# Kernel optimization log

Measured on AMD Instinct MI355X. Metric: run time of the kernel, lower is better.

## Reference

```python
import jax, jax.numpy as jnp
import numpy as np
from jax import lax

DT = 0.01  # fixed Euler-Maruyama step size

B, N, C, M, H, T = 1024, 64, 16, 16, 512, 128


def setup_inputs() -> dict:
    key = jax.random.key(0)
    ks = jax.random.split(key, 8)
    d_in = N + C  # concat(y, control)
    inp = {
        "y0": jax.random.normal(ks[0], (B, N), jnp.float32),
        "controls": jax.random.normal(ks[1], (T, C), jnp.float32),
        "noise": jax.random.normal(ks[2], (T - 1, B, M), jnp.float32),
        # mu MLP: d_in -> H -> N
        "W1_mu": jax.random.normal(ks[3], (d_in, H), jnp.float32) / np.sqrt(d_in),
        "b1_mu": jnp.zeros((H,), jnp.float32),
        "W2_mu": jax.random.normal(ks[4], (H, N), jnp.float32) / np.sqrt(H),
        "b2_mu": jnp.zeros((N,), jnp.float32),
        # sigma MLP: d_in -> H -> N*M
        "W1_sg": jax.random.normal(ks[5], (d_in, H), jnp.float32) / np.sqrt(d_in),
        "b1_sg": jnp.zeros((H,), jnp.float32),
        "W2_sg": jax.random.normal(ks[6], (H, N * M), jnp.float32) / np.sqrt(H),
        "b2_sg": jnp.zeros((N * M,), jnp.float32),
    }
    return inp


def _mlp(x, W1, b1, W2, b2):
    return jnp.maximum(x @ W1 + b1, 0.0) @ W2 + b2


def reference(y0, controls, noise, W1_mu, b1_mu, W2_mu, b2_mu,
              W1_sg, b1_sg, W2_sg, b2_sg):
    """Euler-Maruyama solve of dy = f(y,u) dt + g(y,u) dW.
    Returns trajectory [T, B, N] including y0 (as torchsde.sdeint does)."""
    b, n = y0.shape
    m = noise.shape[-1]
    sqrt_dt = jnp.sqrt(jnp.asarray(DT, y0.dtype))

    def step(y, inp):
        u, z = inp  # u: [C] control at t_k, z: [B, M] standard normal
        x = jnp.concatenate([y, jnp.broadcast_to(u[None, :], (b, u.shape[0]))], axis=1)
        drift = _mlp(x, W1_mu, b1_mu, W2_mu, b2_mu)              # [B, N]
        diff = _mlp(x, W1_sg, b1_sg, W2_sg, b2_sg).reshape(b, n, m)  # [B, N, M]
        dW = z * sqrt_dt
        y_next = y + drift * DT + jnp.einsum('bnm,bm->bn', diff, dW)
        return y_next, y_next

    _, ys = lax.scan(step, y0, (controls[:-1], noise))
    return jnp.concatenate([y0[None], ys], axis=0)  # [T, B, N]
```

## Files before the change

### kernel.cpp

```cpp
#include <hip/hip_runtime.h>


typedef _Float16 f16x8 __attribute__((ext_vector_type(8)));
typedef float    f32x4 __attribute__((ext_vector_type(4)));
typedef float    f32x2 __attribute__((ext_vector_type(2)));

#define MFMA(a,b,c) __builtin_amdgcn_mfma_f32_16x16x32_f16(a,b,c,0,0,0)

#define Bb 1024
#define Tt 128
#define NG 64
#define GB 8
#define Rr 16
#define NT 512
#define CNT_STRIDE 16
#define MAGIC1 0x1234ABCDu
#define MAGIC2 0xFEDC4321u

#define W2SG_OFF 0
#define W2SG_HALVES (64*16*2*512)
#define W2MU_OFF (W2SG_OFF + W2SG_HALVES)
#define W2MU_HALVES (4*16*2*512)
#define W1MU_OFF (W2MU_OFF + W2MU_HALVES)
#define W1_HALVES (32*3*2*512)
#define W1SG_OFF (W1MU_OFF + W1_HALVES)
#define WS_HALVES (W1SG_OFF + W1_HALVES)
#define ACC_BYTES_OFF ((size_t)WS_HALVES * 2)
#define ACC_FLOATS (3 * NG * 1024)
#define CNT_OFF   (ACC_BYTES_OFF + (size_t)ACC_FLOATS*4)
#define DTEST_DW  (NG*GB*16)
#define DW16      (NG*16)
#define DET_DW    (DTEST_DW + 6*DW16)
#define WS_END    (CNT_OFF + (size_t)(DW16 + DET_DW)*4)

__global__ __launch_bounds__(256) void pack_weights(
    const float* __restrict__ W1_mu, const float* __restrict__ W2_mu,
    const float* __restrict__ W1_sg, const float* __restrict__ W2_sg,
    _Float16* __restrict__ wsh)
{
    int gid = blockIdx.x * 256 + threadIdx.x;
    if (gid >= 81920) return;
    const float* src; int ncols, kvalid; size_t dst;
    int id, tile, ks, lane;
    if (gid < 65536) {
        id = gid; tile = id >> 10; id &= 1023; ks = id >> 6; lane = id & 63;
        src = W2_sg; ncols = 1024; kvalid = 512;
        dst = W2SG_OFF + (size_t)((tile*16 + ks)*2) * 512 + lane*8;
    } else if (gid < 69632) {
        id = gid - 65536; tile = id >> 10; id &= 1023; ks = id >> 6; lane = id & 63;
        src = W2_mu; ncols = 64; kvalid = 512;
        dst = W2MU_OFF + (size_t)((tile*16 + ks)*2) * 512 + lane*8;
    } else if (gid < 75776) {
        id = gid - 69632; tile = id / 192; id %= 192; ks = id >> 6; lane = id & 63;
        src = W1_mu; ncols = 512; kvalid = 80;
        dst = W1MU_OFF + (size_t)((tile*3 + ks)*2) * 512 + lane*8;
    } else {
        id = gid - 75776; tile = id / 192; id %= 192; ks = id >> 6; lane = id & 63;
        src = W1_sg; ncols = 512; kvalid = 80;
        dst = W1SG_OFF + (size_t)((tile*3 + ks)*2) * 512 + lane*8;
    }
    const int n  = tile*16 + (lane & 15);
    const int kb = ks*32 + ((lane >> 4) << 3);
    f16x8 hi8, lo8;
    #pragma unroll
    for (int jj = 0; jj < 8; ++jj) {
        int k = kb + jj;
        float wv = (k < kvalid) ? src[(size_t)k * ncols + n] : 0.f;
        _Float16 h = (_Float16)wv;
        hi8[jj] = h;
        lo8[jj] = (_Float16)(wv - (float)h);
    }
    *((f16x8*)(wsh + dst))       = hi8;
    *((f16x8*)(wsh + dst + 512)) = lo8;
}

__device__ __forceinline__ unsigned sc0_load_u32(const unsigned* p) {
    unsigned v;
    asm volatile("global_load_dword %0, %1, off sc0\n\ts_waitcnt vmcnt(0)"
                 : "=v"(v) : "v"((const void*)p) : "memory");
    return v;
}

__global__ __launch_bounds__(NT, 4) void nsde_r9(
    const float* __restrict__ y0, const float* __restrict__ controls,
    const float* __restrict__ noise,
    const float* __restrict__ b1_mu, const float* __restrict__ b2_mu,
    const float* __restrict__ b1_sg, const float* __restrict__ b2_sg,
    const _Float16* __restrict__ wf,
    float* __restrict__ accbuf, unsigned int* __restrict__ cnt,
    float* __restrict__ out)
{
    __shared__ _Float16 s_xhi[Rr][104], s_xlo[Rr][104];
    __shared__ _Float16 s_hhi[2][Rr][72], s_hlo[2][Rr][72];
    __shared__ float s_y[Rr*64];
    __shared__ float s_dw[Rr][16];
    __shared__ float s_part[Rr*64];
    __shared__ float s_pmu[Rr*64];
    __shared__ int   s_mode;

    const int tid  = threadIdx.x;
    const int lane = tid & 63, w = tid >> 6;
    const int m15  = lane & 15, quad = lane >> 4;
    const int g    = blockIdx.x & 63;
    const int j    = blockIdx.x >> 6;
    const int r0   = g * Rr;

    unsigned* dtest = cnt + NG*16;
    unsigned* dcntA = dtest + NG*GB*16;
    unsigned* dcntB = dcntA + NG*16;
    unsigned* dtc   = dcntB + NG*16;
    unsigned* dcntC = dtc   + NG*16;
    unsigned* dok   = dcntC + NG*16;
    unsigned* dcnt2 = dok   + NG*16;

    const int l  = w >> 2;
    const int ct = w & 3;
    const int tg = j*4 + ct;
    const _Float16* w1base = wf + (l ? W1SG_OFF : W1MU_OFF);
    const float bias1 = (l ? b1_sg : b1_mu)[j*64 + ct*16 + m15];
    float b2v[8];
    #pragma unroll
    for (int t = 0; t < 8; ++t)
        b2v[t] = (j == 0) ? b2_sg[(w + t*8)*16 + m15] : 0.f;
    const float b2m = (w < 4 && j == 0) ? b2_mu[w*16 + m15] * 0.01f : 0.f;

    if (tid == 0) {
        volatile unsigned* my = (volatile unsigned*)&dtest[(size_t)(g*GB + j)*16];
        int ok = 1;
        *my = MAGIC1;
        asm volatile("s_waitcnt vmcnt(0)" ::: "memory");
        __hip_atomic_fetch_add(&dcntA[g*16], 1u, __ATOMIC_RELEASE,
                               __HIP_MEMORY_SCOPE_AGENT);
        while (__hip_atomic_load(&dcntA[g*16], __ATOMIC_RELAXED,
                                 __HIP_MEMORY_SCOPE_AGENT) < (unsigned)GB)
            __builtin_amdgcn_s_sleep(2);
        for (int b = 0; b < GB; ++b)
            ok &= (sc0_load_u32(&dtest[(size_t)(g*GB + b)*16]) == MAGIC1);
        *my = MAGIC2;
        asm volatile("s_waitcnt vmcnt(0)" ::: "memory");
        __hip_atomic_fetch_add(&dcntB[g*16], 1u, __ATOMIC_RELEASE,
                               __HIP_MEMORY_SCOPE_AGENT);
        while (__hip_atomic_load(&dcntB[g*16], __ATOMIC_RELAXED,
                                 __HIP_MEMORY_SCOPE_AGENT) < (unsigned)GB)
            __builtin_amdgcn_s_sleep(2);
        for (int b = 0; b < GB; ++b)
            ok &= (sc0_load_u32(&dtest[(size_t)(g*GB + b)*16]) == MAGIC2);
        __hip_atomic_fetch_add(&dtc[g*16], 1u, __ATOMIC_RELAXED,
                               __HIP_MEMORY_SCOPE_WORKGROUP);
        asm volatile("s_waitcnt vmcnt(0)" ::: "memory");
        __hip_atomic_fetch_add(&dcntC[g*16], 1u, __ATOMIC_RELEASE,
                               __HIP_MEMORY_SCOPE_AGENT);
        while (__hip_atomic_load(&dcntC[g*16], __ATOMIC_RELAXED,
                                 __HIP_MEMORY_SCOPE_AGENT) < (unsigned)GB)
            __builtin_amdgcn_s_sleep(2);
        ok &= (sc0_load_u32(&dtc[g*16]) == (unsigned)GB);
        __hip_atomic_fetch_add(&dok[g*16], ok ? 1u : 0u, __ATOMIC_RELEASE,
                               __HIP_MEMORY_SCOPE_AGENT);
        __hip_atomic_fetch_add(&dcnt2[g*16], 1u, __ATOMIC_RELEASE,
                               __HIP_MEMORY_SCOPE_AGENT);
        while (__hip_atomic_load(&dcnt2[g*16], __ATOMIC_RELAXED,
                                 __HIP_MEMORY_SCOPE_AGENT) < (unsigned)GB)
            __builtin_amdgcn_s_sleep(2);
        s_mode = (__hip_atomic_load(&dok[g*16], __ATOMIC_RELAXED,
                                    __HIP_MEMORY_SCOPE_AGENT) == (unsigned)GB);
    }
    __syncthreads();
    const bool local = (s_mode != 0);

    for (int e = tid; e < Rr*24; e += NT) {
        int r = e / 24, c = 80 + e % 24;
        s_xhi[r][c] = (_Float16)0.f; s_xlo[r][c] = (_Float16)0.f;
    }
    if (tid < 256) {
        int e0 = tid*4, r = e0 >> 6, n = e0 & 63;
        float4 yv = *(const float4*)&y0[(size_t)(r0 + r)*64 + n];
        float vv[4] = {yv.x, yv.y, yv.z, yv.w};
        #pragma unroll
        for (int q = 0; q < 4; ++q) {
            s_y[e0+q] = vv[q];
            _Float16 h = (_Float16)vv[q];
            s_xhi[r][n+q] = h; s_xlo[r][n+q] = (_Float16)(vv[q] - (float)h);
        }
        if ((tid >> 5) == j)
            *(float4*)&out[(size_t)(r0 + r)*64 + n] = yv;
        int rr2 = tid >> 4, cc2 = tid & 15;
        float u = controls[cc2];
        _Float16 h = (_Float16)u;
        s_xhi[rr2][64+cc2] = h; s_xlo[rr2][64+cc2] = (_Float16)(u - (float)h);
        s_dw[rr2][cc2] = noise[(size_t)(r0 + rr2)*16 + cc2] * 0.1f;
    }
    __syncthreads();

    for (int k = 0; k < Tt-1; ++k) {
        {
            f32x4 a0 = {0,0,0,0}, a1 = {0,0,0,0}, a2 = {0,0,0,0};
            #pragma unroll
            for (int ks = 0; ks < 3; ++ks) {
                const _Float16* bp = w1base + (size_t)((tg*3 + ks)*2)*512 + lane*8;
                f16x8 bh = *(const f16x8*)bp;
                f16x8 bl = *(const f16x8*)(bp + 512);
                f16x8 ah = *(const f16x8*)&s_xhi[m15][ks*32 + quad*8];
                f16x8 al = *(const f16x8*)&s_xlo[m15][ks*32 + quad*8];
                a0 = MFMA(ah, bh, a0);
                a1 = MFMA(ah, bl, a1);
                a2 = MFMA(al, bh, a2);
            }
            f32x4 s = a0 + a1 + a2;
            #pragma unroll
            for (int rg = 0; rg < 4; ++rg) {
                int row = quad*4 + rg;
                float v = fmaxf(s[rg] + bias1, 0.f);
                _Float16 h = (_Float16)v;
                s_hhi[l][row][ct*16 + m15] = h;
                s_hlo[l][row][ct*16 + m15] = (_Float16)(v - (float)h);
            }
        }
        float u_nx = 0.f, dw_nx = 0.f;
        const int r2 = tid >> 4, c2 = tid & 15;
        if (k < Tt-2 && tid < 256) {
            u_nx  = controls[(size_t)(k+1)*16 + c2];
            dw_nx = noise[((size_t)(k+1)*Bb + r0 + r2)*16 + c2] * 0.1f;
        }
        __syncthreads();

        float dwv[4];
        #pragma unroll
        for (int rg = 0; rg < 4; ++rg)
            dwv[rg] = s_dw[quad*4 + rg][m15];

        if (w < 4) {
            f16x8 Mh0 = *(const f16x8*)&s_hhi[0][m15][quad*8];
            f16x8 Ml0 = *(const f16x8*)&s_hlo[0][m15][quad*8];
            f16x8 Mh1 = *(const f16x8*)&s_hhi[0][m15][32 + quad*8];
            f16x8 Ml1 = *(const f16x8*)&s_hlo[0][m15][32 + quad*8];
            const _Float16* bp = wf + W2MU_OFF + (size_t)((w*16 + 2*j)*2)*512 + lane*8;
            f16x8 bh0 = *(const f16x8*)(bp);
            f16x8 bl0 = *(const f16x8*)(bp + 512);
            f16x8 bh1 = *(const f16x8*)(bp + 1024);
            f16x8 bl1 = *(const f16x8*)(bp + 1536);
            f32x4 hh = {0,0,0,0}, hl = {0,0,0,0}, lh = {0,0,0,0};
            hh = MFMA(Mh0, bh0, hh); hl = MFMA(Mh0, bl0, hl); lh = MFMA(Ml0, bh0, lh);
            hh = MFMA(Mh1, bh1, hh); hl = MFMA(Mh1, bl1, hl); lh = MFMA(Ml1, bh1, lh);
            f32x4 s = hh + hl + lh;
            #pragma unroll
            for (int rg = 0; rg < 4; ++rg)
                s_pmu[(quad*4 + rg)*64 + w*16 + m15] = s[rg]*0.01f + b2m;
        }

        f16x8 Ah0 = *(const f16x8*)&s_hhi[1][m15][quad*8];
        f16x8 Al0 = *(const f16x8*)&s_hlo[1][m15][quad*8];
        f16x8 Ah1 = *(const f16x8*)&s_hhi[1][m15][32 + quad*8];
        f16x8 Al1 = *(const f16x8*)&s_hlo[1][m15][32 + quad*8];
        #pragma unroll 2
        for (int t = 0; t < 8; ++t) {
            const int nt = w + t*8;
            const _Float16* bp = wf + W2SG_OFF + (size_t)((nt*16 + 2*j)*2)*512 + lane*8;
            f16x8 bh0 = *(const f16x8*)(bp);
            f16x8 bl0 = *(const f16x8*)(bp + 512);
            f16x8 bh1 = *(const f16x8*)(bp + 1024);
            f16x8 bl1 = *(const f16x8*)(bp + 1536);
            f32x4 hh = {0,0,0,0}, hl = {0,0,0,0}, lh = {0,0,0,0};
            hh = MFMA(Ah0, bh0, hh); hl = MFMA(Ah0, bl0, hl); lh = MFMA(Al0, bh0, lh);
            hh = MFMA(Ah1, bh1, hh); hl = MFMA(Ah1, bl1, hl); lh = MFMA(Al1, bh1, lh);
            f32x4 s = hh + hl + lh;
            #pragma unroll
            for (int rg = 0; rg < 4; ++rg) {
                float v = (s[rg] + b2v[t]) * dwv[rg];
                v += __shfl_xor(v, 1); v += __shfl_xor(v, 2);
                v += __shfl_xor(v, 4); v += __shfl_xor(v, 8);
                if (m15 == 0) s_part[(quad*4 + rg)*64 + nt] = v;
            }
        }
        __syncthreads();

        const int slot = k % 3;
        float* ab = accbuf + ((size_t)slot*NG + g)*1024;
        const int e0 = tid*2;
        {
            float v0 = s_part[e0]   + s_pmu[e0];
            float v1 = s_part[e0+1] + s_pmu[e0+1];
            if (local) {
                __hip_atomic_fetch_add(&ab[e0],   v0, __ATOMIC_RELAXED,
                                       __HIP_MEMORY_SCOPE_WORKGROUP);
                __hip_atomic_fetch_add(&ab[e0+1], v1, __ATOMIC_RELAXED,
                                       __HIP_MEMORY_SCOPE_WORKGROUP);
            } else {
                __hip_atomic_fetch_add(&ab[e0],   v0, __ATOMIC_RELAXED,
                                       __HIP_MEMORY_SCOPE_AGENT);
                __hip_atomic_fetch_add(&ab[e0+1], v1, __ATOMIC_RELAXED,
                                       __HIP_MEMORY_SCOPE_AGENT);
            }
        }
        __syncthreads();
        if (tid == 0) {
            if (local) {
                __hip_atomic_fetch_add(&cnt[g*CNT_STRIDE], 1u, __ATOMIC_RELEASE,
                                       __HIP_MEMORY_SCOPE_WORKGROUP);
                const unsigned tgt = (unsigned)GB*(k+1);
                for (;;) {
                    unsigned v = sc0_load_u32(&cnt[g*CNT_STRIDE]);
                    if (v >= tgt) break;
                    __builtin_amdgcn_s_sleep(2);
                }
            } else {
                __hip_atomic_fetch_add(&cnt[g*CNT_STRIDE], 1u, __ATOMIC_RELEASE,
                                       __HIP_MEMORY_SCOPE_AGENT);
                while (__hip_atomic_load(&cnt[g*CNT_STRIDE], __ATOMIC_RELAXED,
                                         __HIP_MEMORY_SCOPE_AGENT) < (unsigned)GB*(k+1))
                    __builtin_amdgcn_s_sleep(2);
            }
        }
        __syncthreads();

        {
            const int r = e0 >> 6, n = e0 & 63;
            float sum0, sum1;
            if (local) {
                f32x2 sv;
                asm volatile("global_load_dwordx2 %0, %1, off sc0\n\t"
                             "s_waitcnt vmcnt(0)"
                             : "=v"(sv) : "v"((const void*)&ab[e0]) : "memory");
                sum0 = sv[0]; sum1 = sv[1];
            } else {
                sum0 = __hip_atomic_load(&ab[e0], __ATOMIC_RELAXED,
                                         __HIP_MEMORY_SCOPE_AGENT);
                sum1 = __hip_atomic_load(&ab[e0+1], __ATOMIC_RELAXED,
                                         __HIP_MEMORY_SCOPE_AGENT);
            }
            float ya = s_y[e0]   + sum0;
            float yb = s_y[e0+1] + sum1;
            s_y[e0] = ya; s_y[e0+1] = yb;
            _Float16 ha = (_Float16)ya, hb = (_Float16)yb;
            s_xhi[r][n] = ha;   s_xlo[r][n]   = (_Float16)(ya - (float)ha);
            s_xhi[r][n+1] = hb; s_xlo[r][n+1] = (_Float16)(yb - (float)hb);
            if ((tid >> 6) == j) {
                float2 o = {ya, yb};
                *(float2*)&out[((size_t)(k+1)*Bb + r0 + r)*64 + n] = o;
                if (k >= 1) {
                    float* zb = accbuf + ((size_t)((k-1)%3)*NG + g)*1024;
                    if (local) {
                        *(volatile float*)&zb[e0]   = 0.f;
                        *(volatile float*)&zb[e0+1] = 0.f;
                    } else {
                        __hip_atomic_store(&zb[e0],   0.f, __ATOMIC_RELAXED,
                                           __HIP_MEMORY_SCOPE_AGENT);
                        __hip_atomic_store(&zb[e0+1], 0.f, __ATOMIC_RELAXED,
                                           __HIP_MEMORY_SCOPE_AGENT);
                    }
                }
            }
        }
        if (k < Tt-2 && tid < 256) {
            _Float16 h = (_Float16)u_nx;
            s_xhi[r2][64+c2] = h; s_xlo[r2][64+c2] = (_Float16)(u_nx - (float)h);
            s_dw[r2][c2] = dw_nx;
        }
        __syncthreads();
    }
}

extern "C" void kernel_launch(void* const* d_in, const int* in_sizes, int n_in,
                              void* d_out, int out_size, void* d_ws, size_t ws_size,
                              hipStream_t stream) {
    const float* y0       = (const float*)d_in[0];
    const float* controls = (const float*)d_in[1];
    const float* noise    = (const float*)d_in[2];
    const float* W1_mu    = (const float*)d_in[3];
    const float* b1_mu    = (const float*)d_in[4];
    const float* W2_mu    = (const float*)d_in[5];
    const float* b2_mu    = (const float*)d_in[6];
    const float* W1_sg    = (const float*)d_in[7];
    const float* b1_sg    = (const float*)d_in[8];
    const float* W2_sg    = (const float*)d_in[9];
    const float* b2_sg    = (const float*)d_in[10];
    float* out = (float*)d_out;
    _Float16* wsh = (_Float16*)d_ws;
    float* accbuf = (float*)((char*)d_ws + ACC_BYTES_OFF);
    unsigned int* cnt = (unsigned int*)((char*)d_ws + CNT_OFF);

    hipMemsetAsync((char*)d_ws + ACC_BYTES_OFF, 0,
                   WS_END - ACC_BYTES_OFF, stream);
    pack_weights<<<320, 256, 0, stream>>>(W1_mu, W2_mu, W1_sg, W2_sg, wsh);
    nsde_r9<<<NG*GB, NT, 0, stream>>>(y0, controls, noise,
                                      b1_mu, b2_mu, b1_sg, b2_sg,
                                      (const _Float16*)wsh,
                                      accbuf, cnt, out);
}
```

Baseline: 2.105 ms.

## Keep W1/W2mu fragments in registers and precompute control contribution during barrier wait

```diff
diff --git a/kernel.cpp b/kernel.cpp
--- a/kernel.cpp
+++ b/kernel.cpp
@@ -81,7 +81,7 @@
     return v;
 }
 
-__global__ __launch_bounds__(NT, 4) void nsde_r9(
+__global__ __launch_bounds__(NT, 4) void nsde_r10(
     const float* __restrict__ y0, const float* __restrict__ controls,
     const float* __restrict__ noise,
     const float* __restrict__ b1_mu, const float* __restrict__ b2_mu,
@@ -101,9 +101,10 @@
     const int tid  = threadIdx.x;
     const int lane = tid & 63, w = tid >> 6;
     const int m15  = lane & 15, quad = lane >> 4;
-    const int g    = blockIdx.x & 63;
-    const int j    = blockIdx.x >> 6;
-    const int r0   = g * Rr;
+    const int bx = blockIdx.x;
+    const int g  = (bx & 7) | (((bx >> 3) & 3) << 3) | (((bx >> 8) & 1) << 5);
+    const int j  = (bx >> 5) & 7;
+    const int r0 = g * Rr;
 
     unsigned* dtest = cnt + NG*16;
     unsigned* dcntA = dtest + NG*GB*16;
@@ -123,6 +124,23 @@
     for (int t = 0; t < 8; ++t)
         b2v[t] = (j == 0) ? b2_sg[(w + t*8)*16 + m15] : 0.f;
     const float b2m = (w < 4 && j == 0) ? b2_mu[w*16 + m15] * 0.01f : 0.f;
+
+    f16x8 w1h[3], w1l[3];
+    #pragma unroll
+    for (int ks = 0; ks < 3; ++ks) {
+        const _Float16* bp = w1base + (size_t)((tg*3 + ks)*2)*512 + lane*8;
+        w1h[ks] = *(const f16x8*)bp;
+        w1l[ks] = *(const f16x8*)(bp + 512);
+    }
+    f16x8 wmu[4];
+    {
+        const int wm = w & 3;
+        const _Float16* bp = wf + W2MU_OFF + (size_t)((wm*16 + 2*j)*2)*512 + lane*8;
+        wmu[0] = *(const f16x8*)(bp);
+        wmu[1] = *(const f16x8*)(bp + 512);
+        wmu[2] = *(const f16x8*)(bp + 1024);
+        wmu[3] = *(const f16x8*)(bp + 1536);
+    }
 
     if (tid == 0) {
         volatile unsigned* my = (volatile unsigned*)&dtest[(size_t)(g*GB + j)*16];
@@ -172,12 +190,12 @@
         s_xhi[r][c] = (_Float16)0.f; s_xlo[r][c] = (_Float16)0.f;
     }
     if (tid < 256) {
-        int e0 = tid*4, r = e0 >> 6, n = e0 & 63;
+        int e0i = tid*4, r = e0i >> 6, n = e0i & 63;
         float4 yv = *(const float4*)&y0[(size_t)(r0 + r)*64 + n];
         float vv[4] = {yv.x, yv.y, yv.z, yv.w};
         #pragma unroll
         for (int q = 0; q < 4; ++q) {
-            s_y[e0+q] = vv[q];
+            s_y[e0i+q] = vv[q];
             _Float16 h = (_Float16)vv[q];
             s_xhi[r][n+q] = h; s_xlo[r][n+q] = (_Float16)(vv[q] - (float)h);
         }
@@ -191,19 +209,26 @@
     }
     __syncthreads();
 
+    f32x4 pre0, pre1, pre2;
+    {
+        f16x8 ah = *(const f16x8*)&s_xhi[m15][64 + quad*8];
+        f16x8 al = *(const f16x8*)&s_xlo[m15][64 + quad*8];
+        f32x4 z = {0,0,0,0};
+        pre0 = MFMA(ah, w1h[2], z);
+        pre1 = MFMA(ah, w1l[2], z);
+        pre2 = MFMA(al, w1h[2], z);
+    }
+
     for (int k = 0; k < Tt-1; ++k) {
         {
-            f32x4 a0 = {0,0,0,0}, a1 = {0,0,0,0}, a2 = {0,0,0,0};
+            f32x4 a0 = pre0, a1 = pre1, a2 = pre2;
             #pragma unroll
-            for (int ks = 0; ks < 3; ++ks) {
-                const _Float16* bp = w1base + (size_t)((tg*3 + ks)*2)*512 + lane*8;
-                f16x8 bh = *(const f16x8*)bp;
-                f16x8 bl = *(const f16x8*)(bp + 512);
+            for (int ks = 0; ks < 2; ++ks) {
                 f16x8 ah = *(const f16x8*)&s_xhi[m15][ks*32 + quad*8];
                 f16x8 al = *(const f16x8*)&s_xlo[m15][ks*32 + quad*8];
-                a0 = MFMA(ah, bh, a0);
-                a1 = MFMA(ah, bl, a1);
-                a2 = MFMA(al, bh, a2);
+                a0 = MFMA(ah, w1h[ks], a0);
+                a1 = MFMA(ah, w1l[ks], a1);
+                a2 = MFMA(al, w1h[ks], a2);
             }
             f32x4 s = a0 + a1 + a2;
             #pragma unroll
@@ -233,14 +258,11 @@
             f16x8 Ml0 = *(const f16x8*)&s_hlo[0][m15][quad*8];
             f16x8 Mh1 = *(const f16x8*)&s_hhi[0][m15][32 + quad*8];
             f16x8 Ml1 = *(const f16x8*)&s_hlo[0][m15][32 + quad*8];
-            const _Float16* bp = wf + W2MU_OFF + (size_t)((w*16 + 2*j)*2)*512 + lane*8;
-            f16x8 bh0 = *(const f16x8*)(bp);
-            f16x8 bl0 = *(const f16x8*)(bp + 512);
-            f16x8 bh1 = *(const f16x8*)(bp + 1024);
-            f16x8 bl1 = *(const f16x8*)(bp + 1536);
             f32x4 hh = {0,0,0,0}, hl = {0,0,0,0}, lh = {0,0,0,0};
-            hh = MFMA(Mh0, bh0, hh); hl = MFMA(Mh0, bl0, hl); lh = MFMA(Ml0, bh0, lh);
-            hh = MFMA(Mh1, bh1, hh); hl = MFMA(Mh1, bl1, hl); lh = MFMA(Ml1, bh1, lh);
+            hh = MFMA(Mh0, wmu[0], hh); hl = MFMA(Mh0, wmu[1], hl);
+            lh = MFMA(Ml0, wmu[0], lh);
+            hh = MFMA(Mh1, wmu[2], hh); hl = MFMA(Mh1, wmu[3], hl);
+            lh = MFMA(Ml1, wmu[2], lh);
             f32x4 s = hh + hl + lh;
             #pragma unroll
             for (int rg = 0; rg < 4; ++rg)
@@ -291,22 +313,40 @@
                                        __HIP_MEMORY_SCOPE_AGENT);
             }
         }
+        if (k < Tt-2 && tid < 256) {
+            _Float16 h = (_Float16)u_nx;
+            s_xhi[r2][64+c2] = h; s_xlo[r2][64+c2] = (_Float16)(u_nx - (float)h);
+            s_dw[r2][c2] = dw_nx;
+        }
         __syncthreads();
+
         if (tid == 0) {
-            if (local) {
+            if (local)
                 __hip_atomic_fetch_add(&cnt[g*CNT_STRIDE], 1u, __ATOMIC_RELEASE,
                                        __HIP_MEMORY_SCOPE_WORKGROUP);
-                const unsigned tgt = (unsigned)GB*(k+1);
+            else
+                __hip_atomic_fetch_add(&cnt[g*CNT_STRIDE], 1u, __ATOMIC_RELEASE,
+                                       __HIP_MEMORY_SCOPE_AGENT);
+        }
+        if (k < Tt-2) {
+            f16x8 ah = *(const f16x8*)&s_xhi[m15][64 + quad*8];
+            f16x8 al = *(const f16x8*)&s_xlo[m15][64 + quad*8];
+            f32x4 z = {0,0,0,0};
+            pre0 = MFMA(ah, w1h[2], z);
+            pre1 = MFMA(ah, w1l[2], z);
+            pre2 = MFMA(al, w1h[2], z);
+        }
+        if (tid == 0) {
+            const unsigned tgt = (unsigned)GB*(k+1);
+            if (local) {
                 for (;;) {
                     unsigned v = sc0_load_u32(&cnt[g*CNT_STRIDE]);
                     if (v >= tgt) break;
                     __builtin_amdgcn_s_sleep(2);
                 }
             } else {
-                __hip_atomic_fetch_add(&cnt[g*CNT_STRIDE], 1u, __ATOMIC_RELEASE,
-                                       __HIP_MEMORY_SCOPE_AGENT);
                 while (__hip_atomic_load(&cnt[g*CNT_STRIDE], __ATOMIC_RELAXED,
-                                         __HIP_MEMORY_SCOPE_AGENT) < (unsigned)GB*(k+1))
+                                         __HIP_MEMORY_SCOPE_AGENT) < tgt)
                     __builtin_amdgcn_s_sleep(2);
             }
         }
@@ -336,24 +376,19 @@
             if ((tid >> 6) == j) {
                 float2 o = {ya, yb};
                 *(float2*)&out[((size_t)(k+1)*Bb + r0 + r)*64 + n] = o;
-                if (k >= 1) {
-                    float* zb = accbuf + ((size_t)((k-1)%3)*NG + g)*1024;
-                    if (local) {
-                        *(volatile float*)&zb[e0]   = 0.f;
-                        *(volatile float*)&zb[e0+1] = 0.f;
-                    } else {
-                        __hip_atomic_store(&zb[e0],   0.f, __ATOMIC_RELAXED,
-                                           __HIP_MEMORY_SCOPE_AGENT);
-                        __hip_atomic_store(&zb[e0+1], 0.f, __ATOMIC_RELAXED,
-                                           __HIP_MEMORY_SCOPE_AGENT);
-                    }
+            }
+            if (k >= 1 && (tid >> 6) == ((j+4)&7)) {
+                float* zb = accbuf + ((size_t)((k-1)%3)*NG + g)*1024;
+                if (local) {
+                    *(volatile float*)&zb[e0]   = 0.f;
+                    *(volatile float*)&zb[e0+1] = 0.f;
+                } else {
+                    __hip_atomic_store(&zb[e0],   0.f, __ATOMIC_RELAXED,
+                                       __HIP_MEMORY_SCOPE_AGENT);
+                    __hip_atomic_store(&zb[e0+1], 0.f, __ATOMIC_RELAXED,
+                                       __HIP_MEMORY_SCOPE_AGENT);
                 }
             }
-        }
-        if (k < Tt-2 && tid < 256) {
-            _Float16 h = (_Float16)u_nx;
-            s_xhi[r2][64+c2] = h; s_xlo[r2][64+c2] = (_Float16)(u_nx - (float)h);
-            s_dw[r2][c2] = dw_nx;
         }
         __syncthreads();
     }
@@ -381,8 +416,8 @@
     hipMemsetAsync((char*)d_ws + ACC_BYTES_OFF, 0,
                    WS_END - ACC_BYTES_OFF, stream);
     pack_weights<<<320, 256, 0, stream>>>(W1_mu, W2_mu, W1_sg, W2_sg, wsh);
-    nsde_r9<<<NG*GB, NT, 0, stream>>>(y0, controls, noise,
-                                      b1_mu, b2_mu, b1_sg, b2_sg,
-                                      (const _Float16*)wsh,
-                                      accbuf, cnt, out);
+    nsde_r10<<<NG*GB, NT, 0, stream>>>(y0, controls, noise,
+                                       b1_mu, b2_mu, b1_sg, b2_sg,
+                                       (const _Float16*)wsh,
+                                       accbuf, cnt, out);
 }
```

New measurement: 3.137 ms. 49.0% more time.

## Precompute control-column MFMA of layer one during the inter-block barrier wait

Applied to the files above, without the earlier changes.

```diff
diff --git a/kernel.cpp b/kernel.cpp
--- a/kernel.cpp
+++ b/kernel.cpp
@@ -81,7 +81,7 @@
     return v;
 }
 
-__global__ __launch_bounds__(NT, 4) void nsde_r9(
+__global__ __launch_bounds__(NT, 4) void nsde_r11(
     const float* __restrict__ y0, const float* __restrict__ controls,
     const float* __restrict__ noise,
     const float* __restrict__ b1_mu, const float* __restrict__ b2_mu,
@@ -172,12 +172,12 @@
         s_xhi[r][c] = (_Float16)0.f; s_xlo[r][c] = (_Float16)0.f;
     }
     if (tid < 256) {
-        int e0 = tid*4, r = e0 >> 6, n = e0 & 63;
+        int e0i = tid*4, r = e0i >> 6, n = e0i & 63;
         float4 yv = *(const float4*)&y0[(size_t)(r0 + r)*64 + n];
         float vv[4] = {yv.x, yv.y, yv.z, yv.w};
         #pragma unroll
         for (int q = 0; q < 4; ++q) {
-            s_y[e0+q] = vv[q];
+            s_y[e0i+q] = vv[q];
             _Float16 h = (_Float16)vv[q];
             s_xhi[r][n+q] = h; s_xlo[r][n+q] = (_Float16)(vv[q] - (float)h);
         }
@@ -191,11 +191,24 @@
     }
     __syncthreads();
 
+    f32x4 pre0, pre1, pre2;
+    {
+        const _Float16* bp = w1base + (size_t)((tg*3 + 2)*2)*512 + lane*8;
+        f16x8 bh = *(const f16x8*)bp;
+        f16x8 bl = *(const f16x8*)(bp + 512);
+        f16x8 ah = *(const f16x8*)&s_xhi[m15][64 + quad*8];
+        f16x8 al = *(const f16x8*)&s_xlo[m15][64 + quad*8];
+        f32x4 z = {0,0,0,0};
+        pre0 = MFMA(ah, bh, z);
+        pre1 = MFMA(ah, bl, z);
+        pre2 = MFMA(al, bh, z);
+    }
+
     for (int k = 0; k < Tt-1; ++k) {
         {
-            f32x4 a0 = {0,0,0,0}, a1 = {0,0,0,0}, a2 = {0,0,0,0};
+            f32x4 a0 = pre0, a1 = pre1, a2 = pre2;
             #pragma unroll
-            for (int ks = 0; ks < 3; ++ks) {
+            for (int ks = 0; ks < 2; ++ks) {
                 const _Float16* bp = w1base + (size_t)((tg*3 + ks)*2)*512 + lane*8;
                 f16x8 bh = *(const f16x8*)bp;
                 f16x8 bl = *(const f16x8*)(bp + 512);
@@ -291,22 +304,43 @@
                                        __HIP_MEMORY_SCOPE_AGENT);
             }
         }
+        if (k < Tt-2 && tid < 256) {
+            _Float16 h = (_Float16)u_nx;
+            s_xhi[r2][64+c2] = h; s_xlo[r2][64+c2] = (_Float16)(u_nx - (float)h);
+            s_dw[r2][c2] = dw_nx;
+        }
         __syncthreads();
+
         if (tid == 0) {
-            if (local) {
+            if (local)
                 __hip_atomic_fetch_add(&cnt[g*CNT_STRIDE], 1u, __ATOMIC_RELEASE,
                                        __HIP_MEMORY_SCOPE_WORKGROUP);
-                const unsigned tgt = (unsigned)GB*(k+1);
+            else
+                __hip_atomic_fetch_add(&cnt[g*CNT_STRIDE], 1u, __ATOMIC_RELEASE,
+                                       __HIP_MEMORY_SCOPE_AGENT);
+        }
+        if (k < Tt-2) {
+            const _Float16* bp = w1base + (size_t)((tg*3 + 2)*2)*512 + lane*8;
+            f16x8 bh = *(const f16x8*)bp;
+            f16x8 bl = *(const f16x8*)(bp + 512);
+            f16x8 ah = *(const f16x8*)&s_xhi[m15][64 + quad*8];
+            f16x8 al = *(const f16x8*)&s_xlo[m15][64 + quad*8];
+            f32x4 z = {0,0,0,0};
+            pre0 = MFMA(ah, bh, z);
+            pre1 = MFMA(ah, bl, z);
+            pre2 = MFMA(al, bh, z);
+        }
+        if (tid == 0) {
+            const unsigned tgt = (unsigned)GB*(k+1);
+            if (local) {
                 for (;;) {
                     unsigned v = sc0_load_u32(&cnt[g*CNT_STRIDE]);
                     if (v >= tgt) break;
                     __builtin_amdgcn_s_sleep(2);
                 }
             } else {
-                __hip_atomic_fetch_add(&cnt[g*CNT_STRIDE], 1u, __ATOMIC_RELEASE,
-                                       __HIP_MEMORY_SCOPE_AGENT);
                 while (__hip_atomic_load(&cnt[g*CNT_STRIDE], __ATOMIC_RELAXED,
-                                         __HIP_MEMORY_SCOPE_AGENT) < (unsigned)GB*(k+1))
+                                         __HIP_MEMORY_SCOPE_AGENT) < tgt)
                     __builtin_amdgcn_s_sleep(2);
             }
         }
@@ -336,24 +370,19 @@
             if ((tid >> 6) == j) {
                 float2 o = {ya, yb};
                 *(float2*)&out[((size_t)(k+1)*Bb + r0 + r)*64 + n] = o;
-                if (k >= 1) {
-                    float* zb = accbuf + ((size_t)((k-1)%3)*NG + g)*1024;
-                    if (local) {
-                        *(volatile float*)&zb[e0]   = 0.f;
-                        *(volatile float*)&zb[e0+1] = 0.f;
-                    } else {
-                        __hip_atomic_store(&zb[e0],   0.f, __ATOMIC_RELAXED,
-                                           __HIP_MEMORY_SCOPE_AGENT);
-                        __hip_atomic_store(&zb[e0+1], 0.f, __ATOMIC_RELAXED,
-                                           __HIP_MEMORY_SCOPE_AGENT);
-                    }
+            }
+            if (k >= 1 && (tid >> 6) == ((j+4)&7)) {
+                float* zb = accbuf + ((size_t)((k-1)%3)*NG + g)*1024;
+                if (local) {
+                    *(volatile float*)&zb[e0]   = 0.f;
+                    *(volatile float*)&zb[e0+1] = 0.f;
+                } else {
+                    __hip_atomic_store(&zb[e0],   0.f, __ATOMIC_RELAXED,
+                                       __HIP_MEMORY_SCOPE_AGENT);
+                    __hip_atomic_store(&zb[e0+1], 0.f, __ATOMIC_RELAXED,
+                                       __HIP_MEMORY_SCOPE_AGENT);
                 }
             }
-        }
-        if (k < Tt-2 && tid < 256) {
-            _Float16 h = (_Float16)u_nx;
-            s_xhi[r2][64+c2] = h; s_xlo[r2][64+c2] = (_Float16)(u_nx - (float)h);
-            s_dw[r2][c2] = dw_nx;
         }
         __syncthreads();
     }
@@ -381,8 +410,8 @@
     hipMemsetAsync((char*)d_ws + ACC_BYTES_OFF, 0,
                    WS_END - ACC_BYTES_OFF, stream);
     pack_weights<<<320, 256, 0, stream>>>(W1_mu, W2_mu, W1_sg, W2_sg, wsh);
-    nsde_r9<<<NG*GB, NT, 0, stream>>>(y0, controls, noise,
-                                      b1_mu, b2_mu, b1_sg, b2_sg,
-                                      (const _Float16*)wsh,
-                                      accbuf, cnt, out);
+    nsde_r11<<<NG*GB, NT, 0, stream>>>(y0, controls, noise,
+                                       b1_mu, b2_mu, b1_sg, b2_sg,
+                                       (const _Float16*)wsh,
+                                       accbuf, cnt, out);
 }
```

Measured after the change: 2.547 ms. 21.0% more time.
